# Kernel tuning notes

Measured on AMD Instinct MI355X. Metric: run time of the kernel, lower is better.

## Reference

```python
import jax, jax.numpy as jnp
import numpy as np
from jax import lax

EPS = 1e-5

def _layernorm_c(x, w, b):
    # WithBias LayerNorm over channel dim (to_3d puts C last; equivalent to axis=1 here)
    mu = x.mean(axis=1, keepdims=True)
    var = x.var(axis=1, keepdims=True)
    return (x - mu) / jnp.sqrt(var + EPS) * w[None, :, None, None] + b[None, :, None, None]

def _conv1x1(x, W, b=None):
    y = jnp.einsum('bchw,oc->bohw', x, W)
    if b is not None:
        y = y + b[None, :, None, None]
    return y

def _dwconv3x3(x, k):
    # k: [C, 1, 3, 3], groups = C
    return lax.conv_general_dilated(
        x, k, window_strides=(1, 1), padding='SAME',
        dimension_numbers=('NCHW', 'OIHW', 'NCHW'),
        feature_group_count=k.shape[0])

def setup_inputs() -> dict:
    key = jax.random.key(0)
    B, C, H, W = 4, 128, 96, 256
    ks = jax.random.split(key, 12)
    s = 0.05
    return {
        'x_l': jax.random.normal(ks[0], (B, C, H, W), jnp.float32),
        'x_r': jax.random.normal(ks[1], (B, C, H, W), jnp.float32),
        'Wl_m': jax.random.normal(ks[2], (2 * C, C), jnp.float32) * s,
        'Wr_m': jax.random.normal(ks[3], (2 * C, C), jnp.float32) * s,
        'dw_l': jax.random.normal(ks[4], (2 * C, 1, 3, 3), jnp.float32) * s,
        'dw_r': jax.random.normal(ks[5], (2 * C, 1, 3, 3), jnp.float32) * s,
        'lnl_w': jnp.ones((C,), jnp.float32),
        'lnl_b': jnp.zeros((C,), jnp.float32),
        'lnr_w': jnp.ones((C,), jnp.float32),
        'lnr_b': jnp.zeros((C,), jnp.float32),
        'Wq_l': jax.random.normal(ks[6], (C, C), jnp.float32) * s,
        'bq_l': jnp.zeros((C,), jnp.float32),
        'Wq_r': jax.random.normal(ks[7], (C, C), jnp.float32) * s,
        'bq_r': jnp.zeros((C,), jnp.float32),
        'beta': jax.random.normal(ks[8], (1, C, 1, 1), jnp.float32) * s,
        'gamma': jax.random.normal(ks[9], (1, C, 1, 1), jnp.float32) * s,
    }

def reference(x_l, x_r, Wl_m, Wr_m, dw_l, dw_r, lnl_w, lnl_b, lnr_w, lnr_b,
              Wq_l, bq_l, Wq_r, bq_r, beta, gamma):
    c = x_l.shape[1]
    scale = c ** -0.5
    fusion_l = _dwconv3x3(_conv1x1(x_l, Wl_m), dw_l)   # [b,2c,h,w]
    V_l, l_mid = jnp.split(fusion_l, 2, axis=1)
    fusion_r = _dwconv3x3(_conv1x1(x_r, Wr_m), dw_r)
    V_r, r_mid = jnp.split(fusion_r, 2, axis=1)
    Q_l = _conv1x1(_layernorm_c(l_mid, lnl_w, lnl_b), Wq_l, bq_l)  # [b,c,h,w]
    Q_r = _conv1x1(_layernorm_c(r_mid, lnr_w, lnr_b), Wq_r, bq_r)  # [b,c,h,w]
    # row-wise attention over width: [b,h,w,w]
    attn = jnp.einsum('bchw,bchv->bhwv', Q_l, Q_r) * scale
    # F_r2l: softmax over last axis (v), contract V_r over v
    F_r2l = jnp.einsum('bhwv,bchv->bchw', jax.nn.softmax(attn, axis=-1), V_r)
    # F_l2r: softmax of attn^T over its last axis == softmax over w (axis=-2)
    F_l2r = jnp.einsum('bhwv,bchw->bchv', jax.nn.softmax(attn, axis=-2), V_l)
    out_l = x_l + F_r2l * beta
    out_r = x_r + F_l2r * gamma
    return (out_l, out_r)
```

## Files before the change

kernel.cpp:

```cpp
#include <hip/hip_runtime.h>
#include <hip/hip_bf16.h>

using bf16 = __hip_bfloat16;
typedef __attribute__((ext_vector_type(8))) short bf16x8;
typedef __attribute__((ext_vector_type(2))) float f32x2;
typedef __attribute__((ext_vector_type(4))) float f32x4;
typedef __attribute__((ext_vector_type(16))) float f32x16;
typedef __attribute__((ext_vector_type(4))) unsigned int u32x4;

#define DEVI __device__ __forceinline__

constexpr int B = 4, C = 128, C2 = 256, H = 96, W = 256;
constexpr int HW = H * W;
constexpr int NPIX = B * HW;
constexpr int BH = B * H;
constexpr float SCALE = 0.08838834764831845f;
constexpr float LN_EPS = 1e-5f;

DEVI float lo16(unsigned u) { return __builtin_bit_cast(float, u << 16); }
DEVI float hi16(unsigned u) { return __builtin_bit_cast(float, u & 0xffff0000u); }
DEVI unsigned short f2bu(float v) {
    bf16 b = __float2bfloat16(v);
    return __builtin_bit_cast(unsigned short, b);
}
DEVI unsigned packbf2(float a, float b) {
    return (unsigned)f2bu(a) | ((unsigned)f2bu(b) << 16);
}
DEVI f32x2 up2(unsigned p) { return f32x2{lo16(p), hi16(p)}; }

__global__ __launch_bounds__(256) void wcvt_kernel(
    const float* __restrict__ w0, const float* __restrict__ w1,
    const float* __restrict__ w2, const float* __restrict__ w3,
    unsigned short* __restrict__ o0, unsigned short* __restrict__ o1,
    unsigned short* __restrict__ o2, unsigned short* __restrict__ o3)
{
    const int id = blockIdx.x, t = threadIdx.x;
    const float* src; unsigned short* dst; int base;
    if (id < 8)       { src = w0; dst = o0; base = id * 4096; }
    else if (id < 16) { src = w1; dst = o1; base = (id - 8) * 4096; }
    else if (id < 20) { src = w2; dst = o2; base = (id - 16) * 4096; }
    else              { src = w3; dst = o3; base = (id - 20) * 4096; }
#pragma unroll
    for (int u = 0; u < 4; ++u) {
        int i = base + t * 16 + u * 4;
        float4 v = *reinterpret_cast<const float4*>(&src[i]);
        ushort4 o;
        o.x = f2bu(v.x); o.y = f2bu(v.y); o.z = f2bu(v.z); o.w = f2bu(v.w);
        *reinterpret_cast<ushort4*>(&dst[i]) = o;
    }
}

__global__ __launch_bounds__(256) void conv1x1_mfma_kernel(
    const float* __restrict__ x_l, const float* __restrict__ x_r,
    const unsigned short* __restrict__ Wb_l, const unsigned short* __restrict__ Wb_r,
    unsigned short* __restrict__ y_l, unsigned short* __restrict__ y_r)
{
    __shared__ unsigned char xs[64 * 256];
    const int side = blockIdx.x & 1;
    const int u = blockIdx.x >> 1;
    const float* x = side ? x_r : x_l;
    const unsigned short* Wb = side ? Wb_r : Wb_l;
    unsigned short* y = side ? y_r : y_l;

    const int t = threadIdx.x;
    const int b = u / (HW / 64);
    const int hw0 = (u % (HW / 64)) * 64;

    const int lane = t & 63, wid = t >> 6;
    const int l15 = lane & 15, l4 = lane >> 4;

    bf16x8 wfrag[4][4];
#pragma unroll
    for (int kk = 0; kk < 4; ++kk)
#pragma unroll
        for (int nt = 0; nt < 4; ++nt)
            wfrag[kk][nt] = *reinterpret_cast<const bf16x8*>(
                &Wb[(size_t)(wid * 64 + nt * 16 + l15) * C + kk * 32 + l4 * 8]);

    {
        const int px4 = (t & 15) * 4;
        const int c8 = (t >> 4) * 8;
        float v_[8][4];
#pragma unroll
        for (int j = 0; j < 8; ++j) {
            float4 v = *reinterpret_cast<const float4*>(
                &x[((size_t)b * C + c8 + j) * HW + hw0 + px4]);
            v_[j][0] = v.x; v_[j][1] = v.y; v_[j][2] = v.z; v_[j][3] = v.w;
        }
#pragma unroll
        for (int i = 0; i < 4; ++i) {
            const int px = px4 + i;
            uint4 o;
            o.x = packbf2(v_[0][i], v_[1][i]);
            o.y = packbf2(v_[2][i], v_[3][i]);
            o.z = packbf2(v_[4][i], v_[5][i]);
            o.w = packbf2(v_[6][i], v_[7][i]);
            const unsigned addr =
                (unsigned)(px * 256) + (((unsigned)(c8 * 2)) ^ (unsigned)((px & 7) << 4));
            *reinterpret_cast<uint4*>(xs + addr) = o;
        }
    }
    __syncthreads();

    f32x4 acc[4][4] = {};
#pragma unroll
    for (int kk = 0; kk < 4; ++kk) {
        const int k0b = (kk * 32 + l4 * 8) * 2;
        bf16x8 a[4];
#pragma unroll
        for (int mt = 0; mt < 4; ++mt) {
            const int pxl = mt * 16 + l15;
            const unsigned aaddr =
                (unsigned)(pxl * 256) + (((unsigned)k0b) ^ (unsigned)((pxl & 7) << 4));
            a[mt] = *reinterpret_cast<const bf16x8*>(xs + aaddr);
        }
#pragma unroll
        for (int mt = 0; mt < 4; ++mt)
#pragma unroll
            for (int nt = 0; nt < 4; ++nt)
                acc[mt][nt] = __builtin_amdgcn_mfma_f32_16x16x32_bf16(
                    wfrag[kk][nt], a[mt], acc[mt][nt], 0, 0, 0);
    }
#pragma unroll
    for (int mt = 0; mt < 4; ++mt) {
        const size_t px = (size_t)(b * HW + hw0 + mt * 16 + l15);
#pragma unroll
        for (int nt = 0; nt < 4; ++nt) {
            const int oc = wid * 64 + nt * 16 + l4 * 4;
            uint2 o;
            o.x = packbf2(acc[mt][nt][0], acc[mt][nt][1]);
            o.y = packbf2(acc[mt][nt][2], acc[mt][nt][3]);
            *reinterpret_cast<uint2*>(&y[px * C2 + oc]) = o;
        }
    }
}

__global__ __launch_bounds__(128) void dwv_kernel(
    const unsigned short* __restrict__ y_l, const unsigned short* __restrict__ y_r,
    const float* __restrict__ dwk_l, const float* __restrict__ dwk_r,
    unsigned short* __restrict__ VT_l, unsigned short* __restrict__ VT_r)
{
    const int side = blockIdx.x & 1;
    const int u = blockIdx.x >> 1;
    const unsigned short* y = side ? y_r : y_l;
    const float* dwk = side ? dwk_r : dwk_l;
    unsigned short* VT = side ? VT_r : VT_l;

    const int t = threadIdx.x;
    const int wt = u & 3;
    const int bh = u >> 2;
    const int h = bh % H;
    const int ch8 = t & 15, wi = t >> 4;
    const int c0 = ch8 * 8;
    const int wbase = wt * 64 + wi * 8;

    f32x2 acc2[8][4] = {};
#pragma unroll
    for (int dh = 0; dh < 3; ++dh) {
        const int hh = h + dh - 1;
        if ((unsigned)hh >= (unsigned)H) continue;
        f32x2 wt0[4], wt1[4], wt2[4];
#pragma unroll
        for (int k = 0; k < 4; ++k) {
            const float* d0 = dwk + (c0 + 2 * k) * 9 + dh * 3;
            const float* d1 = dwk + (c0 + 2 * k + 1) * 9 + dh * 3;
            wt0[k] = f32x2{d0[0], d1[0]};
            wt1[k] = f32x2{d0[1], d1[1]};
            wt2[k] = f32x2{d0[2], d1[2]};
        }
        const unsigned short* yrow = y + (size_t)(bh + dh - 1) * W * C2 + c0;
        uint4 uu[10];
#pragma unroll
        for (int j = 0; j < 10; ++j) {
            const int ww = wbase - 1 + j;
            uint4 v = {0u, 0u, 0u, 0u};
            if ((unsigned)ww < 256u)
                v = *reinterpret_cast<const uint4*>(&yrow[(size_t)ww * C2]);
            uu[j] = v;
        }
#pragma unroll
        for (int j = 0; j < 10; ++j) {
            const unsigned arr[4] = {uu[j].x, uu[j].y, uu[j].z, uu[j].w};
            f32x2 v[4];
#pragma unroll
            for (int k = 0; k < 4; ++k) v[k] = up2(arr[k]);
            if (j < 8) {
#pragma unroll
                for (int k = 0; k < 4; ++k) acc2[j][k] += v[k] * wt0[k];
            }
            if (j >= 1 && j <= 8) {
#pragma unroll
                for (int k = 0; k < 4; ++k) acc2[j - 1][k] += v[k] * wt1[k];
            }
            if (j >= 2) {
#pragma unroll
                for (int k = 0; k < 4; ++k) acc2[j - 2][k] += v[k] * wt2[k];
            }
        }
    }
#pragma unroll
    for (int k = 0; k < 8; ++k) {
        uint4 o;
        o.x = packbf2(acc2[0][k >> 1][k & 1], acc2[1][k >> 1][k & 1]);
        o.y = packbf2(acc2[2][k >> 1][k & 1], acc2[3][k >> 1][k & 1]);
        o.z = packbf2(acc2[4][k >> 1][k & 1], acc2[5][k >> 1][k & 1]);
        o.w = packbf2(acc2[6][k >> 1][k & 1], acc2[7][k >> 1][k & 1]);
        *reinterpret_cast<uint4*>(&VT[((size_t)bh * C + c0 + k) * W + wbase]) = o;
    }
}

__global__ __launch_bounds__(128) void dwmid_kernel(
    const unsigned short* __restrict__ y_l, const unsigned short* __restrict__ y_r,
    const float* __restrict__ dwk_l, const float* __restrict__ dwk_r,
    const float* __restrict__ lnw_l, const float* __restrict__ lnb_l,
    const float* __restrict__ lnw_r, const float* __restrict__ lnb_r,
    const unsigned short* __restrict__ Wq_l, const unsigned short* __restrict__ Wq_r,
    const float* __restrict__ bq_l, const float* __restrict__ bq_r,
    unsigned short* __restrict__ q_l, unsigned short* __restrict__ q_r)
{
    __shared__ unsigned char msb[64 * 256];
    __shared__ float lnwb[256];

    const int side = blockIdx.x & 1;
    const int u = blockIdx.x >> 1;
    const unsigned short* y = side ? y_r : y_l;
    const float* dwk = side ? dwk_r : dwk_l;
    const float* lnw = side ? lnw_r : lnw_l;
    const float* lnb = side ? lnb_r : lnb_l;
    const unsigned short* Wqb = side ? Wq_r : Wq_l;
    const float* bq = side ? bq_r : bq_l;
    unsigned short* q = side ? q_r : q_l;

    const int t = threadIdx.x;
    const int wt = u & 3;
    const int bh = u >> 2;
    const int h = bh % H;
    const int ch8 = t & 15, wi = t >> 4;
    const int c0m = ch8 * 8;
    const int wbase = wt * 64 + wi * 8;

    lnwb[t] = lnw[t];
    lnwb[t + 128] = lnb[t];

    f32x2 acc2[8][4] = {};
#pragma unroll
    for (int dh = 0; dh < 3; ++dh) {
        const int hh = h + dh - 1;
        if ((unsigned)hh >= (unsigned)H) continue;
        f32x2 wt0[4], wt1[4], wt2[4];
#pragma unroll
        for (int k = 0; k < 4; ++k) {
            const float* d0 = dwk + (128 + c0m + 2 * k) * 9 + dh * 3;
            const float* d1 = dwk + (128 + c0m + 2 * k + 1) * 9 + dh * 3;
            wt0[k] = f32x2{d0[0], d1[0]};
            wt1[k] = f32x2{d0[1], d1[1]};
            wt2[k] = f32x2{d0[2], d1[2]};
        }
        const unsigned short* yrow = y + (size_t)(bh + dh - 1) * W * C2 + 128 + c0m;
        uint4 uu[10];
#pragma unroll
        for (int j = 0; j < 10; ++j) {
            const int ww = wbase - 1 + j;
            uint4 v = {0u, 0u, 0u, 0u};
            if ((unsigned)ww < 256u)
                v = *reinterpret_cast<const uint4*>(&yrow[(size_t)ww * C2]);
            uu[j] = v;
        }
#pragma unroll
        for (int j = 0; j < 10; ++j) {
            const unsigned arr[4] = {uu[j].x, uu[j].y, uu[j].z, uu[j].w};
            f32x2 v[4];
#pragma unroll
            for (int k = 0; k < 4; ++k) v[k] = up2(arr[k]);
            if (j < 8) {
#pragma unroll
                for (int k = 0; k < 4; ++k) acc2[j][k] += v[k] * wt0[k];
            }
            if (j >= 1 && j <= 8) {
#pragma unroll
                for (int k = 0; k < 4; ++k) acc2[j - 1][k] += v[k] * wt1[k];
            }
            if (j >= 2) {
#pragma unroll
                for (int k = 0; k < 4; ++k) acc2[j - 2][k] += v[k] * wt2[k];
            }
        }
    }

#pragma unroll
    for (int i = 0; i < 8; ++i) {
        uint4 o;
        o.x = packbf2(acc2[i][0].x, acc2[i][0].y);
        o.y = packbf2(acc2[i][1].x, acc2[i][1].y);
        o.z = packbf2(acc2[i][2].x, acc2[i][2].y);
        o.w = packbf2(acc2[i][3].x, acc2[i][3].y);
        const int pxl = wi * 8 + i;
        const unsigned addr =
            (unsigned)(pxl * 256 + c0m * 2) ^ (unsigned)((pxl & 7) << 4);
        *reinterpret_cast<uint4*>(msb + addr) = o;
    }
    __syncthreads();

    {
        const int px = t >> 1, qq = t & 1;
        uint4 raw[8];
#pragma unroll
        for (int v = 0; v < 8; ++v) {
            const unsigned addr =
                (unsigned)(px * 256 + qq * 128 + v * 16) ^ (unsigned)((px & 7) << 4);
            raw[v] = *reinterpret_cast<const uint4*>(msb + addr);
        }
        float s1 = 0.f, s2 = 0.f;
#pragma unroll
        for (int v = 0; v < 8; ++v) {
            const unsigned arr[4] = {raw[v].x, raw[v].y, raw[v].z, raw[v].w};
#pragma unroll
            for (int k = 0; k < 4; ++k) {
                float v0 = lo16(arr[k]), v1 = hi16(arr[k]);
                s1 += v0 + v1; s2 += v0 * v0 + v1 * v1;
            }
        }
        s1 += __shfl_xor(s1, 1); s2 += __shfl_xor(s2, 1);
        const float mu = s1 * (1.f / C);
        const float rs = rsqrtf(s2 * (1.f / C) - mu * mu + LN_EPS);
#pragma unroll
        for (int v = 0; v < 8; ++v) {
            const unsigned arr[4] = {raw[v].x, raw[v].y, raw[v].z, raw[v].w};
            float nv[8];
#pragma unroll
            for (int k = 0; k < 4; ++k) {
                int c = qq * 64 + v * 8 + k * 2;
                nv[k * 2]     = (lo16(arr[k]) - mu) * rs * lnwb[c] + lnwb[128 + c];
                nv[k * 2 + 1] = (hi16(arr[k]) - mu) * rs * lnwb[c + 1] + lnwb[128 + c + 1];
            }
            uint4 wv;
            wv.x = packbf2(nv[0], nv[1]); wv.y = packbf2(nv[2], nv[3]);
            wv.z = packbf2(nv[4], nv[5]); wv.w = packbf2(nv[6], nv[7]);
            const unsigned addr =
                (unsigned)(px * 256 + qq * 128 + v * 16) ^ (unsigned)((px & 7) << 4);
            *reinterpret_cast<uint4*>(msb + addr) = wv;
        }
    }
    __syncthreads();

    {
        const int lane = t & 63, wid = t >> 6;
        const int l15 = lane & 15, l4 = lane >> 4;
        f32x4 acc[2][8] = {};
        for (int kk = 0; kk < 4; ++kk) {
            const int k0 = kk * 32 + l4 * 8;
            bf16x8 a[2];
#pragma unroll
            for (int pt = 0; pt < 2; ++pt) {
                const int pxl = (wid * 2 + pt) * 16 + l15;
                const unsigned aaddr =
                    (unsigned)(pxl * 256 + k0 * 2) ^ (unsigned)((pxl & 7) << 4);
                a[pt] = *reinterpret_cast<const bf16x8*>(msb + aaddr);
            }
#pragma unroll
            for (int nt = 0; nt < 8; ++nt) {
                bf16x8 bv = *reinterpret_cast<const bf16x8*>(
                    &Wqb[(size_t)(nt * 16 + l15) * C + k0]);
#pragma unroll
                for (int pt = 0; pt < 2; ++pt)
                    acc[pt][nt] = __builtin_amdgcn_mfma_f32_16x16x32_bf16(bv, a[pt], acc[pt][nt], 0, 0, 0);
            }
        }
        const size_t px0 = (size_t)bh * W + wt * 64;
#pragma unroll
        for (int pt = 0; pt < 2; ++pt) {
            const size_t px = px0 + (wid * 2 + pt) * 16 + l15;
#pragma unroll
            for (int nt = 0; nt < 8; ++nt) {
                const int oc = nt * 16 + l4 * 4;
                const float4 bias = *reinterpret_cast<const float4*>(&bq[oc]);
                uint2 o;
                o.x = packbf2(acc[pt][nt][0] + bias.x, acc[pt][nt][1] + bias.y);
                o.y = packbf2(acc[pt][nt][2] + bias.z, acc[pt][nt][3] + bias.w);
                *reinterpret_cast<uint2*>(&q[px * C + oc]) = o;
            }
        }
    }
}

__global__ __launch_bounds__(256, 2) void fused_attn_kernel(
    const unsigned short* __restrict__ Q_l, const unsigned short* __restrict__ Q_r,
    const unsigned short* __restrict__ VT_l, const unsigned short* __restrict__ VT_r,
    const float* __restrict__ x_l, const float* __restrict__ x_r,
    const float* __restrict__ beta, const float* __restrict__ gamma,
    float* __restrict__ out_l, float* __restrict__ out_r)
{
    __shared__ __align__(16) unsigned char lds[65536];
    const int bid = blockIdx.x;
    const int xcd = bid & 7;
    const int local = bid >> 3;
    const int bh = xcd * 48 + (local >> 2);
    const int sub = local & 3;
    const int side = sub & 1, half = sub >> 1;

    const unsigned short* Q  = side ? Q_r : Q_l;
    const unsigned short* K  = side ? Q_l : Q_r;
    const unsigned short* VT = side ? VT_l : VT_r;
    const float* x    = side ? x_r : x_l;
    const float* coef = side ? gamma : beta;
    float* out        = side ? out_r : out_l;

    const int t = threadIdx.x;
    const int lane = t & 63, wv = t >> 6;
    const int l31 = lane & 31, hi = lane >> 5;
    const int b = bh / H, h = bh % H;
    const int w0 = half * 128 + wv * 32;

    const unsigned short* qrow = Q + ((size_t)bh * W + w0 + l31) * C + hi * 8;
    bf16x8 qfrag[8];
#pragma unroll
    for (int ks = 0; ks < 8; ++ks)
        qfrag[ks] = *reinterpret_cast<const bf16x8*>(qrow + ks * 16);

    const char* kg = (const char*)(K + (size_t)bh * W * C);
    const char* vg = (const char*)(VT + (size_t)bh * C * W);
    const int srow = lane >> 4;
    const int scol = (lane & 15) * 16;

    float sden_loc = 0.f;
    f32x16 oacc[4] = {};

    for (int ci = 0; ci < 2; ++ci) {
#pragma unroll
        for (int i = 0; i < 8; ++i) {
            const int r0 = wv * 32 + i * 4;
            const int row = r0 + srow;
            const char* src = kg + (size_t)(ci * 128 + row) * 256 + (scol ^ ((row & 7) << 4));
            __builtin_amdgcn_global_load_lds(
                (const __attribute__((address_space(1))) void*)src,
                (__attribute__((address_space(3))) void*)(lds + r0 * 256), 16, 0, 0);
        }
#pragma unroll
        for (int i = 0; i < 8; ++i) {
            const int r0 = wv * 32 + i * 4;
            const int row = r0 + srow;
            const char* src = vg + (size_t)row * 512 + ci * 256 + (scol ^ ((row & 7) << 4));
            __builtin_amdgcn_global_load_lds(
                (const __attribute__((address_space(1))) void*)src,
                (__attribute__((address_space(3))) void*)(lds + 32768 + r0 * 256), 16, 0, 0);
        }
        __syncthreads();

        f32x16 sacc[4] = {};
        __builtin_amdgcn_s_setprio(1);
#pragma unroll
        for (int vt = 0; vt < 4; ++vt) {
            const int row = vt * 32 + l31;
            const unsigned rb = row * 256;
            const unsigned sw = (row & 7) << 4;
#pragma unroll
            for (int ks = 0; ks < 8; ++ks) {
                bf16x8 a = *reinterpret_cast<const bf16x8*>(
                    lds + rb + ((ks * 32 + hi * 16) ^ sw));
                sacc[vt] = __builtin_amdgcn_mfma_f32_32x32x16_bf16(a, qfrag[ks], sacc[vt], 0, 0, 0);
            }
        }
        __builtin_amdgcn_s_setprio(0);

#pragma unroll
        for (int vt = 0; vt < 4; ++vt)
#pragma unroll
            for (int r = 0; r < 16; ++r) {
                float e = __expf(sacc[vt][r] * SCALE);
                sacc[vt][r] = e;
                sden_loc += e;
            }

        unsigned pw[8][4];
#pragma unroll
        for (int g = 0; g < 8; ++g) {
            const int vt = g >> 1, bs = (g & 1) * 8;
            unsigned pa = packbf2(sacc[vt][bs + 0], sacc[vt][bs + 1]);
            unsigned pc = packbf2(sacc[vt][bs + 2], sacc[vt][bs + 3]);
            unsigned pb = packbf2(sacc[vt][bs + 4], sacc[vt][bs + 5]);
            unsigned pd = packbf2(sacc[vt][bs + 6], sacc[vt][bs + 7]);
            unsigned sa = __shfl_xor(pa, 32);
            unsigned sb = __shfl_xor(pb, 32);
            unsigned sc = __shfl_xor(pc, 32);
            unsigned sd = __shfl_xor(pd, 32);
            pw[g][0] = hi ? sb : pa;
            pw[g][1] = hi ? sd : pc;
            pw[g][2] = hi ? pb : sa;
            pw[g][3] = hi ? pd : sc;
        }

        __builtin_amdgcn_s_setprio(1);
#pragma unroll
        for (int ct = 0; ct < 4; ++ct) {
            const int row = ct * 32 + l31;
            const unsigned rb = 32768 + row * 256;
            const unsigned sw = (row & 7) << 4;
#pragma unroll
            for (int g = 0; g < 8; ++g) {
                bf16x8 va = *reinterpret_cast<const bf16x8*>(
                    lds + rb + ((g * 32 + hi * 16) ^ sw));
                u32x4 pv = {pw[g][0], pw[g][1], pw[g][2], pw[g][3]};
                oacc[ct] = __builtin_amdgcn_mfma_f32_32x32x16_bf16(
                    va, __builtin_bit_cast(bf16x8, pv), oacc[ct], 0, 0, 0);
            }
        }
        __builtin_amdgcn_s_setprio(0);
        __syncthreads();
    }

    const float sden = sden_loc + __shfl_xor(sden_loc, 32);
    const float inv = 1.f / sden;
    const size_t base0 = (size_t)b * C * HW + (size_t)h * W + w0 + l31;
#pragma unroll
    for (int ct = 0; ct < 4; ++ct)
#pragma unroll
        for (int r = 0; r < 16; ++r) {
            const int c = ct * 32 + (r & 3) + 8 * (r >> 2) + 4 * hi;
            const size_t a = base0 + (size_t)c * HW;
            out[a] = x[a] + oacc[ct][r] * inv * coef[c];
        }
}

extern "C" void kernel_launch(void* const* d_in, const int* in_sizes, int n_in,
                              void* d_out, int out_size, void* d_ws, size_t ws_size,
                              hipStream_t stream) {
    (void)in_sizes; (void)n_in; (void)out_size; (void)ws_size;
    const float* x_l   = (const float*)d_in[0];
    const float* x_r   = (const float*)d_in[1];
    const float* Wl_m  = (const float*)d_in[2];
    const float* Wr_m  = (const float*)d_in[3];
    const float* dw_l  = (const float*)d_in[4];
    const float* dw_r  = (const float*)d_in[5];
    const float* lnl_w = (const float*)d_in[6];
    const float* lnl_b = (const float*)d_in[7];
    const float* lnr_w = (const float*)d_in[8];
    const float* lnr_b = (const float*)d_in[9];
    const float* Wq_l  = (const float*)d_in[10];
    const float* bq_l  = (const float*)d_in[11];
    const float* Wq_r  = (const float*)d_in[12];
    const float* bq_r  = (const float*)d_in[13];
    const float* beta  = (const float*)d_in[14];
    const float* gamma = (const float*)d_in[15];

    char* ws = (char*)d_ws;
    unsigned short* ymid_l   = (unsigned short*)(ws + 0);
    unsigned short* ymid_r   = (unsigned short*)(ws + 50331648);
    unsigned short* VT_l     = (unsigned short*)(ws + 150994944);
    unsigned short* VT_r     = (unsigned short*)(ws + 176160768);
    unsigned short* Q_l      = (unsigned short*)(ws + 201326592);
    unsigned short* Q_r      = (unsigned short*)(ws + 226492416);
    unsigned short* Wlb      = (unsigned short*)(ws + 251658240);
    unsigned short* Wrb      = (unsigned short*)(ws + 251723776);
    unsigned short* Wqlb     = (unsigned short*)(ws + 251789312);
    unsigned short* Wqrb     = (unsigned short*)(ws + 251822080);

    float* out_l = (float*)d_out;
    float* out_r = out_l + (size_t)B * C * HW;

    const dim3 blk(256);

    wcvt_kernel<<<24, blk, 0, stream>>>(Wl_m, Wr_m, Wq_l, Wq_r, Wlb, Wrb, Wqlb, Wqrb);

    conv1x1_mfma_kernel<<<3072, blk, 0, stream>>>(x_l, x_r, Wlb, Wrb, ymid_l, ymid_r);
    dwv_kernel<<<3072, dim3(128), 0, stream>>>(ymid_l, ymid_r, dw_l, dw_r, VT_l, VT_r);
    dwmid_kernel<<<3072, dim3(128), 0, stream>>>(ymid_l, ymid_r, dw_l, dw_r,
                                                 lnl_w, lnl_b, lnr_w, lnr_b,
                                                 Wqlb, Wqrb, bq_l, bq_r, Q_l, Q_r);
    fused_attn_kernel<<<1536, blk, 0, stream>>>(Q_l, Q_r, VT_l, VT_r,
                                                x_l, x_r, beta, gamma, out_l, out_r);
}
```

Measured before the change: 228.2 us.

## Process four pixel tiles per conv1x1 block with double-buffered LDS prefetch

The 1x1 conv kernel now handles four 64-pixel tiles per block instead of one, and the grid shrinks from 3072 to 768 blocks. Weight fragments are loaded once per block and reused across the tiles. While the MFMAs run on the current tile, the next tile's global loads are issued into registers and then written to a second LDS buffer. This amortises weight loads and overlaps global latency with compute, at the cost of doubled LDS, more registers, and fewer blocks to spread across CUs.

```diff
diff --git a/kernel.cpp b/kernel.cpp
--- a/kernel.cpp
+++ b/kernel.cpp
@@ -55,7 +55,7 @@
     const unsigned short* __restrict__ Wb_l, const unsigned short* __restrict__ Wb_r,
     unsigned short* __restrict__ y_l, unsigned short* __restrict__ y_r)
 {
-    __shared__ unsigned char xs[64 * 256];
+    __shared__ unsigned char xs[2][64 * 256];
     const int side = blockIdx.x & 1;
     const int u = blockIdx.x >> 1;
     const float* x = side ? x_r : x_l;
@@ -63,11 +63,13 @@
     unsigned short* y = side ? y_r : y_l;
 
     const int t = threadIdx.x;
-    const int b = u / (HW / 64);
-    const int hw0 = (u % (HW / 64)) * 64;
+    const int b = (u * 256) / HW;
+    const int hw_base = (u * 256) % HW;
 
     const int lane = t & 63, wid = t >> 6;
     const int l15 = lane & 15, l4 = lane >> 4;
+    const int px4 = (t & 15) * 4;
+    const int c8 = (t >> 4) * 8;
 
     bf16x8 wfrag[4][4];
 #pragma unroll
@@ -77,62 +79,81 @@
             wfrag[kk][nt] = *reinterpret_cast<const bf16x8*>(
                 &Wb[(size_t)(wid * 64 + nt * 16 + l15) * C + kk * 32 + l4 * 8]);
 
-    {
-        const int px4 = (t & 15) * 4;
-        const int c8 = (t >> 4) * 8;
-        float v_[8][4];
-#pragma unroll
-        for (int j = 0; j < 8; ++j) {
-            float4 v = *reinterpret_cast<const float4*>(
-                &x[((size_t)b * C + c8 + j) * HW + hw0 + px4]);
-            v_[j][0] = v.x; v_[j][1] = v.y; v_[j][2] = v.z; v_[j][3] = v.w;
-        }
-#pragma unroll
-        for (int i = 0; i < 4; ++i) {
-            const int px = px4 + i;
-            uint4 o;
-            o.x = packbf2(v_[0][i], v_[1][i]);
-            o.y = packbf2(v_[2][i], v_[3][i]);
-            o.z = packbf2(v_[4][i], v_[5][i]);
-            o.w = packbf2(v_[6][i], v_[7][i]);
-            const unsigned addr =
-                (unsigned)(px * 256) + (((unsigned)(c8 * 2)) ^ (unsigned)((px & 7) << 4));
-            *reinterpret_cast<uint4*>(xs + addr) = o;
-        }
-    }
+    float v_[8][4];
+
+#define LOADX(tile)                                                         \
+    {                                                                       \
+        _Pragma("unroll")                                                   \
+        for (int j = 0; j < 8; ++j) {                                       \
+            float4 v = *reinterpret_cast<const float4*>(                    \
+                &x[((size_t)b * C + c8 + j) * HW + hw_base + (tile) * 64 + px4]); \
+            v_[j][0] = v.x; v_[j][1] = v.y; v_[j][2] = v.z; v_[j][3] = v.w; \
+        }                                                                   \
+    }
+
+#define WRITELDS(bf)                                                        \
+    {                                                                       \
+        _Pragma("unroll")                                                   \
+        for (int i = 0; i < 4; ++i) {                                       \
+            const int px = px4 + i;                                         \
+            uint4 o;                                                        \
+            o.x = packbf2(v_[0][i], v_[1][i]);                              \
+            o.y = packbf2(v_[2][i], v_[3][i]);                              \
+            o.z = packbf2(v_[4][i], v_[5][i]);                              \
+            o.w = packbf2(v_[6][i], v_[7][i]);                              \
+            const unsigned addr = (unsigned)(px * 256) +                    \
+                (((unsigned)(c8 * 2)) ^ (unsigned)((px & 7) << 4));         \
+            *reinterpret_cast<uint4*>(xs[bf] + addr) = o;                   \
+        }                                                                   \
+    }
+
+    LOADX(0);
+    WRITELDS(0);
     __syncthreads();
 
-    f32x4 acc[4][4] = {};
-#pragma unroll
-    for (int kk = 0; kk < 4; ++kk) {
-        const int k0b = (kk * 32 + l4 * 8) * 2;
-        bf16x8 a[4];
+    for (int tile = 0; tile < 4; ++tile) {
+        const int buf = tile & 1;
+        if (tile < 3) LOADX(tile + 1);
+
+        f32x4 acc[4][4] = {};
+#pragma unroll
+        for (int kk = 0; kk < 4; ++kk) {
+            const int k0b = (kk * 32 + l4 * 8) * 2;
+            bf16x8 a[4];
+#pragma unroll
+            for (int mt = 0; mt < 4; ++mt) {
+                const int pxl = mt * 16 + l15;
+                const unsigned aaddr = (unsigned)(pxl * 256) +
+                    (((unsigned)k0b) ^ (unsigned)((pxl & 7) << 4));
+                a[mt] = *reinterpret_cast<const bf16x8*>(xs[buf] + aaddr);
+            }
+#pragma unroll
+            for (int mt = 0; mt < 4; ++mt)
+#pragma unroll
+                for (int nt = 0; nt < 4; ++nt)
+                    acc[mt][nt] = __builtin_amdgcn_mfma_f32_16x16x32_bf16(
+                        wfrag[kk][nt], a[mt], acc[mt][nt], 0, 0, 0);
+        }
 #pragma unroll
         for (int mt = 0; mt < 4; ++mt) {
-            const int pxl = mt * 16 + l15;
-            const unsigned aaddr =
-                (unsigned)(pxl * 256) + (((unsigned)k0b) ^ (unsigned)((pxl & 7) << 4));
-            a[mt] = *reinterpret_cast<const bf16x8*>(xs + aaddr);
-        }
-#pragma unroll
-        for (int mt = 0; mt < 4; ++mt)
-#pragma unroll
-            for (int nt = 0; nt < 4; ++nt)
-                acc[mt][nt] = __builtin_amdgcn_mfma_f32_16x16x32_bf16(
-                    wfrag[kk][nt], a[mt], acc[mt][nt], 0, 0, 0);
-    }
-#pragma unroll
-    for (int mt = 0; mt < 4; ++mt) {
-        const size_t px = (size_t)(b * HW + hw0 + mt * 16 + l15);
-#pragma unroll
-        for (int nt = 0; nt < 4; ++nt) {
-            const int oc = wid * 64 + nt * 16 + l4 * 4;
-            uint2 o;
-            o.x = packbf2(acc[mt][nt][0], acc[mt][nt][1]);
-            o.y = packbf2(acc[mt][nt][2], acc[mt][nt][3]);
-            *reinterpret_cast<uint2*>(&y[px * C2 + oc]) = o;
-        }
-    }
+            const size_t px = (size_t)(b * HW + hw_base + tile * 64 + mt * 16 + l15);
+#pragma unroll
+            for (int nt = 0; nt < 4; ++nt) {
+                const int oc = wid * 64 + nt * 16 + l4 * 4;
+                uint2 o;
+                o.x = packbf2(acc[mt][nt][0], acc[mt][nt][1]);
+                o.y = packbf2(acc[mt][nt][2], acc[mt][nt][3]);
+                *reinterpret_cast<uint2*>(&y[px * C2 + oc]) = o;
+            }
+        }
+
+        if (tile < 3) {
+            WRITELDS(buf ^ 1);
+            __syncthreads();
+        }
+    }
+#undef LOADX
+#undef WRITELDS
 }
 
 __global__ __launch_bounds__(128) void dwv_kernel(
@@ -561,7 +582,7 @@
 
     wcvt_kernel<<<24, blk, 0, stream>>>(Wl_m, Wr_m, Wq_l, Wq_r, Wlb, Wrb, Wqlb, Wqrb);
 
-    conv1x1_mfma_kernel<<<3072, blk, 0, stream>>>(x_l, x_r, Wlb, Wrb, ymid_l, ymid_r);
+    conv1x1_mfma_kernel<<<768, blk, 0, stream>>>(x_l, x_r, Wlb, Wrb, ymid_l, ymid_r);
     dwv_kernel<<<3072, dim3(128), 0, stream>>>(ymid_l, ymid_r, dw_l, dw_r, VT_l, VT_r);
     dwmid_kernel<<<3072, dim3(128), 0, stream>>>(ymid_l, ymid_r, dw_l, dw_r,
                                                  lnl_w, lnl_b, lnr_w, lnr_b,
```

New measurement: 217.9 us. 4.5% less time.
